# Kernel tuning notes

Hardware: AMD Instinct MI355X
Metric: run time of the kernel (lower is better)

## Reference

```python
import jax, jax.numpy as jnp
import numpy as np

B, N, K, D = 8, 4096, 26, 64


def setup_inputs() -> dict:
    key = jax.random.key(0)
    ks = jax.random.split(key, 7)
    return {
        "targets": jax.random.normal(ks[0], (B, N, D), dtype=jnp.float32),
        "neighbors": jax.random.normal(ks[1], (B, N, K, D), dtype=jnp.float32),
        "a": jax.random.uniform(ks[2], (B, N, K), dtype=jnp.float32),
        "kernel_target": jax.random.normal(ks[3], (1, 1, D), dtype=jnp.float32) * 0.1,
        "bias_target": jax.random.normal(ks[4], (1, 1, D), dtype=jnp.float32) * 0.1,
        "kernel_neighbor": jax.random.normal(ks[5], (1, 1, D), dtype=jnp.float32) * 0.1,
        "bias_neighbor": jax.random.normal(ks[6], (1, 1, 1, D), dtype=jnp.float32) * 0.1,
    }


def reference(targets, neighbors, a, kernel_target, bias_target, kernel_neighbor, bias_neighbor):
    # Faithful to the TF call(), including the broadcast quirk:
    # targets (B,N,D) * kernel_neighbor (1,1,D) + bias_neighbor (1,1,1,D) -> (1,B,N,D)
    t = targets * kernel_neighbor + bias_neighbor            # (1,B,N,D)
    n = neighbors * kernel_target + bias_target              # (B,N,K,D)
    # expand_dims(t, -2) -> (1,B,N,1,D); product with n and a[...,None] -> (1,B,N,K,D);
    # reduce_sum over axis=2 (the N axis of the rank-5 tensor) -> (1,B,K,D).
    # Expressed as a fused einsum to avoid materializing the rank-5 intermediate.
    w = jnp.einsum("zbnd,bnkd,bnk->zbkd", t, n, a)           # (1,B,K,D)
    return jax.nn.sigmoid(w)
```

## Files before the change

### kernel.cpp

```cpp
#include <hip/hip_runtime.h>
#include <math.h>

#define BB 8
#define NN 4096
#define KK 26
#define DD 64
#define CH 128
#define NPB (NN / CH)
#define KD (KK * DD)

__global__ __launch_bounds__(256) void gat_partial_ws(
    const float* __restrict__ targets,
    const float* __restrict__ neighbors,
    const float* __restrict__ a,
    const float* __restrict__ kt, const float* __restrict__ bt,
    const float* __restrict__ kn, const float* __restrict__ bn,
    float* __restrict__ ws)
{
    const int b     = blockIdx.x / CH;
    const int chunk = blockIdx.x % CH;
    const int tid   = threadIdx.x;
    const int wave  = tid >> 6;
    const int lane  = tid & 63;

    const int g16 = lane >> 4, r16 = lane & 15;
    const int g32 = lane >> 5, r32 = lane & 31;

    const float4 kt4 = ((const float4*)kt)[r16];
    const float4 bt4 = ((const float4*)bt)[r16];
    const float4 kn4 = ((const float4*)kn)[r16];
    const float4 bn4 = ((const float4*)bn)[r16];
    const float2 kt2 = ((const float2*)kt)[r32];
    const float2 bt2 = ((const float2*)bt)[r32];
    const float2 kn2 = ((const float2*)kn)[r32];
    const float2 bn2 = ((const float2*)bn)[r32];

    float4 acc4[6];
#pragma unroll
    for (int kk = 0; kk < 6; ++kk) acc4[kk] = make_float4(0.f, 0.f, 0.f, 0.f);
    float2 accT = make_float2(0.f, 0.f);

    const int n0 = chunk * NPB;
    for (int n = n0 + wave; n < n0 + NPB; n += 4) {
        const size_t row = (size_t)(b * NN + n);
        const float4 t4 = ((const float4*)(targets + row * DD))[r16];
        const float2 t2 = ((const float2*)(targets + row * DD))[r32];
        float4 tt4;
        tt4.x = fmaf(t4.x, kn4.x, bn4.x);
        tt4.y = fmaf(t4.y, kn4.y, bn4.y);
        tt4.z = fmaf(t4.z, kn4.z, bn4.z);
        tt4.w = fmaf(t4.w, kn4.w, bn4.w);
        float2 tt2;
        tt2.x = fmaf(t2.x, kn2.x, bn2.x);
        tt2.y = fmaf(t2.y, kn2.y, bn2.y);

        const float4* __restrict__ nbrow4 = (const float4*)(neighbors + row * (size_t)KD);
        const float*  __restrict__ arow   = a + row * KK;
#pragma unroll
        for (int kk = 0; kk < 6; ++kk) {
            const float  av = arow[kk * 4 + g16];
            const float4 v  = nbrow4[kk * 64 + lane];
            acc4[kk].x = fmaf(tt4.x * av, fmaf(v.x, kt4.x, bt4.x), acc4[kk].x);
            acc4[kk].y = fmaf(tt4.y * av, fmaf(v.y, kt4.y, bt4.y), acc4[kk].y);
            acc4[kk].z = fmaf(tt4.z * av, fmaf(v.z, kt4.z, bt4.z), acc4[kk].z);
            acc4[kk].w = fmaf(tt4.w * av, fmaf(v.w, kt4.w, bt4.w), acc4[kk].w);
        }
        {
            const float  av = arow[24 + g32];
            const float2 v  = ((const float2*)nbrow4)[768 + lane];
            accT.x = fmaf(tt2.x * av, fmaf(v.x, kt2.x, bt2.x), accT.x);
            accT.y = fmaf(tt2.y * av, fmaf(v.y, kt2.y, bt2.y), accT.y);
        }
    }

    __shared__ float lds[4][KD];
#pragma unroll
    for (int kk = 0; kk < 6; ++kk)
        ((float4*)lds[wave])[kk * 64 + lane] = acc4[kk];
    ((float2*)lds[wave])[768 + lane] = accT;
    __syncthreads();

    float4* __restrict__ wrow4 = (float4*)(ws + ((size_t)b * CH + chunk) * KD);
    for (int i4 = tid; i4 < KD / 4; i4 += 256) {
        const float4 v0 = ((const float4*)lds[0])[i4];
        const float4 v1 = ((const float4*)lds[1])[i4];
        const float4 v2 = ((const float4*)lds[2])[i4];
        const float4 v3 = ((const float4*)lds[3])[i4];
        float4 s;
        s.x = (v0.x + v1.x) + (v2.x + v3.x);
        s.y = (v0.y + v1.y) + (v2.y + v3.y);
        s.z = (v0.z + v1.z) + (v2.z + v3.z);
        s.w = (v0.w + v1.w) + (v2.w + v3.w);
        wrow4[i4] = s;
    }
}

__global__ __launch_bounds__(256) void gat_reduce_sigmoid(
    const float* __restrict__ ws, float* __restrict__ out)
{
    const int i = blockIdx.x * 256 + threadIdx.x;
    const int total = BB * (KD / 4);
    if (i >= total) return;
    const int b = i / (KD / 4);
    const int j = i % (KD / 4);
    const float4* __restrict__ wsb = (const float4*)(ws + (size_t)b * CH * KD) + j;
    float4 s = make_float4(0.f, 0.f, 0.f, 0.f);
#pragma unroll 4
    for (int c = 0; c < CH; ++c) {
        const float4 v = wsb[(size_t)c * (KD / 4)];
        s.x += v.x; s.y += v.y; s.z += v.z; s.w += v.w;
    }
    float4 o;
    o.x = 1.f / (1.f + expf(-s.x));
    o.y = 1.f / (1.f + expf(-s.y));
    o.z = 1.f / (1.f + expf(-s.z));
    o.w = 1.f / (1.f + expf(-s.w));
    ((float4*)out)[i] = o;
}

__global__ __launch_bounds__(256) void gat_partial_atomic(
    const float* __restrict__ targets, const float* __restrict__ neighbors,
    const float* __restrict__ a,
    const float* __restrict__ kt, const float* __restrict__ bt,
    const float* __restrict__ kn, const float* __restrict__ bn,
    float* __restrict__ out)
{
    const int b     = blockIdx.x / CH;
    const int chunk = blockIdx.x % CH;
    const int tid   = threadIdx.x;
    const int wave  = tid >> 6;
    const int lane  = tid & 63;
    const int d     = lane;
    const float kt_d = kt[d], bt_d = bt[d], kn_d = kn[d], bn_d = bn[d];
    float acc[KK];
#pragma unroll
    for (int k = 0; k < KK; ++k) acc[k] = 0.f;
    const int n0 = chunk * NPB;
    for (int n = n0 + wave; n < n0 + NPB; n += 4) {
        const size_t row = (size_t)(b * NN + n);
        const float tt = fmaf(targets[row * DD + d], kn_d, bn_d);
        const float* __restrict__ nbrow = neighbors + row * (size_t)KD;
        const float* __restrict__ arow  = a + row * KK;
#pragma unroll
        for (int k = 0; k < KK; ++k)
            acc[k] = fmaf(tt * arow[k], fmaf(nbrow[k * DD + d], kt_d, bt_d), acc[k]);
    }
    __shared__ float lds[4][KD];
#pragma unroll
    for (int k = 0; k < KK; ++k) lds[wave][k * DD + lane] = acc[k];
    __syncthreads();
    for (int idx = tid; idx < KD; idx += 256) {
        const float s = lds[0][idx] + lds[1][idx] + lds[2][idx] + lds[3][idx];
        atomicAdd(&out[b * KD + idx], s);
    }
}

__global__ __launch_bounds__(256) void gat_sigmoid(float* __restrict__ out, int nelem) {
    const int i = blockIdx.x * blockDim.x + threadIdx.x;
    if (i < nelem) out[i] = 1.f / (1.f + expf(-out[i]));
}

extern "C" void kernel_launch(void* const* d_in, const int* in_sizes, int n_in,
                              void* d_out, int out_size, void* d_ws, size_t ws_size,
                              hipStream_t stream) {
    const float* targets   = (const float*)d_in[0];
    const float* neighbors = (const float*)d_in[1];
    const float* a         = (const float*)d_in[2];
    const float* kt        = (const float*)d_in[3];
    const float* bt        = (const float*)d_in[4];
    const float* kn        = (const float*)d_in[5];
    const float* bn        = (const float*)d_in[6];
    float* out = (float*)d_out;

    const size_t ws_need = (size_t)BB * CH * KD * sizeof(float);
    if (ws_size >= ws_need) {
        float* ws = (float*)d_ws;
        gat_partial_ws<<<BB * CH, 256, 0, stream>>>(targets, neighbors, a, kt, bt, kn, bn, ws);
        gat_reduce_sigmoid<<<(BB * (KD / 4) + 255) / 256, 256, 0, stream>>>(ws, out);
    } else {
        hipMemsetAsync(d_out, 0, (size_t)out_size * sizeof(float), stream);
        gat_partial_atomic<<<BB * CH, 256, 0, stream>>>(targets, neighbors, a, kt, bt, kn, bn, out);
        gat_sigmoid<<<(out_size + 255) / 256, 256, 0, stream>>>(out, out_size);
    }
}
```

Measured before the change: 51.61 us.

## Fuse partial reduction and sigmoid via atomics and last-block counter

Replaces the per-chunk workspace write plus separate reduce/sigmoid kernel with atomicAdd accumulation into a small per-batch buffer. A per-batch counter identifies the last finishing block, which applies the sigmoid and writes the output. This removes the second kernel launch and the large workspace write/read, but adds a memset, heavy atomic contention (128 blocks per address), and nondeterministic float summation order.

New measurement: 112.7 us. 2.18x slower.

```diff
diff --git a/kernel.cpp b/kernel.cpp
--- a/kernel.cpp
+++ b/kernel.cpp
@@ -8,14 +8,20 @@
 #define CH 128
 #define NPB (NN / CH)
 #define KD (KK * DD)
+#define KD4 (KD / 4)
 
-__global__ __launch_bounds__(256) void gat_partial_ws(
+#define WS_ACC_FLOATS (BB * KD)
+#define WS_BYTES (WS_ACC_FLOATS * 4 + BB * 4)
+
+__global__ __launch_bounds__(256) void gat_fused(
     const float* __restrict__ targets,
     const float* __restrict__ neighbors,
     const float* __restrict__ a,
     const float* __restrict__ kt, const float* __restrict__ bt,
     const float* __restrict__ kn, const float* __restrict__ bn,
-    float* __restrict__ ws)
+    float* __restrict__ ws_acc,
+    int*   __restrict__ ws_cnt,
+    float* __restrict__ out)
 {
     const int b     = blockIdx.x / CH;
     const int chunk = blockIdx.x % CH;
@@ -80,42 +86,25 @@
     ((float2*)lds[wave])[768 + lane] = accT;
     __syncthreads();
 
-    float4* __restrict__ wrow4 = (float4*)(ws + ((size_t)b * CH + chunk) * KD);
-    for (int i4 = tid; i4 < KD / 4; i4 += 256) {
-        const float4 v0 = ((const float4*)lds[0])[i4];
-        const float4 v1 = ((const float4*)lds[1])[i4];
-        const float4 v2 = ((const float4*)lds[2])[i4];
-        const float4 v3 = ((const float4*)lds[3])[i4];
-        float4 s;
-        s.x = (v0.x + v1.x) + (v2.x + v3.x);
-        s.y = (v0.y + v1.y) + (v2.y + v3.y);
-        s.z = (v0.z + v1.z) + (v2.z + v3.z);
-        s.w = (v0.w + v1.w) + (v2.w + v3.w);
-        wrow4[i4] = s;
+    const int bkd = b * KD;
+    for (int idx = tid; idx < KD; idx += 256) {
+        const float s = (lds[0][idx] + lds[1][idx]) + (lds[2][idx] + lds[3][idx]);
+        atomicAdd(&ws_acc[bkd + idx], s);
     }
-}
 
-__global__ __launch_bounds__(256) void gat_reduce_sigmoid(
-    const float* __restrict__ ws, float* __restrict__ out)
-{
-    const int i = blockIdx.x * 256 + threadIdx.x;
-    const int total = BB * (KD / 4);
-    if (i >= total) return;
-    const int b = i / (KD / 4);
-    const int j = i % (KD / 4);
-    const float4* __restrict__ wsb = (const float4*)(ws + (size_t)b * CH * KD) + j;
-    float4 s = make_float4(0.f, 0.f, 0.f, 0.f);
-#pragma unroll 4
-    for (int c = 0; c < CH; ++c) {
-        const float4 v = wsb[(size_t)c * (KD / 4)];
-        s.x += v.x; s.y += v.y; s.z += v.z; s.w += v.w;
+    __threadfence();
+    __shared__ int lastflag;
+    if (tid == 0)
+        lastflag = (atomicAdd(&ws_cnt[b], 1) == CH - 1);
+    __syncthreads();
+
+    if (lastflag) {
+        __threadfence();
+        for (int idx = tid; idx < KD; idx += 256) {
+            const float v = atomicAdd(&ws_acc[bkd + idx], 0.0f);
+            out[bkd + idx] = 1.f / (1.f + expf(-v));
+        }
     }
-    float4 o;
-    o.x = 1.f / (1.f + expf(-s.x));
-    o.y = 1.f / (1.f + expf(-s.y));
-    o.z = 1.f / (1.f + expf(-s.z));
-    o.w = 1.f / (1.f + expf(-s.w));
-    ((float4*)out)[i] = o;
 }
 
 __global__ __launch_bounds__(256) void gat_partial_atomic(
@@ -172,11 +161,12 @@
     const float* bn        = (const float*)d_in[6];
     float* out = (float*)d_out;
 
-    const size_t ws_need = (size_t)BB * CH * KD * sizeof(float);
-    if (ws_size >= ws_need) {
-        float* ws = (float*)d_ws;
-        gat_partial_ws<<<BB * CH, 256, 0, stream>>>(targets, neighbors, a, kt, bt, kn, bn, ws);
-        gat_reduce_sigmoid<<<(BB * (KD / 4) + 255) / 256, 256, 0, stream>>>(ws, out);
+    if (ws_size >= (size_t)WS_BYTES) {
+        float* ws_acc = (float*)d_ws;
+        int*   ws_cnt = (int*)((char*)d_ws + WS_ACC_FLOATS * 4);
+        hipMemsetAsync(d_ws, 0, WS_BYTES, stream);
+        gat_fused<<<BB * CH, 256, 0, stream>>>(targets, neighbors, a, kt, bt, kn, bn,
+                                               ws_acc, ws_cnt, out);
     } else {
         hipMemsetAsync(d_out, 0, (size_t)out_size * sizeof(float), stream);
         gat_partial_atomic<<<BB * CH, 256, 0, stream>>>(targets, neighbors, a, kt, bt, kn, bn, out);
```
